# Optimization experiments

Hardware: AMD Instinct MI355X
Metric: run time of the kernel (lower is better)

The kernel has to match this reference:

```python
import jax, jax.numpy as jnp
import numpy as np


def setup_inputs() -> dict:
    key = jax.random.key(0)
    k1, k2 = jax.random.split(key)
    B, Q, P, D = 4, 75, 5, 640  # episodes, queries, prototypes (5-way), feat dim (ResNet-12)
    return {
        "query_feat": jax.random.normal(k1, (B, Q, D), dtype=jnp.float32),
        "proto_feat": jax.random.normal(k2, (B, P, D), dtype=jnp.float32),
    }


def reference(query_feat, proto_feat):
    # Kendall rank correlation (default mode of ProtoLayer).
    # c_pair = combinations(range(D), 2); x[:, c_pair].diff(-1).sign() ==
    # sign(x[..., j] - x[..., i]) for all i < j.
    D = query_feat.shape[-1]
    i_idx, j_idx = np.triu_indices(D, k=1)  # same order as itertools.combinations
    n_pairs = i_idx.shape[0]  # D*(D-1)/2
    q_rank = jnp.sign(query_feat[..., j_idx] - query_feat[..., i_idx])  # (B, Q, n_pairs)
    s_rank = jnp.sign(proto_feat[..., j_idx] - proto_feat[..., i_idx])  # (B, P, n_pairs)
    # per-batch: query_prank @ support_prank.T / n_pairs -> (B, Q, P)
    return jnp.einsum("bqn,bpn->bqp", q_rank, s_rank) / n_pairs
```

## Files before the change

### kernel.cpp

```cpp
#include <hip/hip_runtime.h>
#include <stdint.h>


#define BB 4
#define QQ 75
#define PP 5
#define DD 640
#define NPAIRS 204480
#define NGROUPS 110
#define NROWS_P 20
#define GPW 5

__device__ __forceinline__ void pack_bit(unsigned& w, float xi_t, float xj) {
    asm("v_cmp_lt_f32 vcc, %1, %2\n\t"
        "v_addc_co_u32 %0, vcc, %0, %0, vcc"
        : "+v"(w)
        : "s"(xi_t), "v"(xj)
        : "vcc");
}

__device__ __forceinline__ unsigned pack_word(const float* __restrict__ xi,
                                              float xj, int dlo, int lane) {
    unsigned w0 = 0, w1 = 0, w2 = 0, w3 = 0;
#pragma unroll
    for (int t = 0; t < 8; ++t) {
        pack_bit(w0, xi[t],      xj);
        pack_bit(w1, xi[t + 8],  xj);
        pack_bit(w2, xi[t + 16], xj);
        pack_bit(w3, xi[t + 24], xj);
    }
    unsigned w = (w0 << 24) | (w1 << 16) | (w2 << 8) | w3;
    if (dlo >= 0) {
        const int n = lane - dlo;
        const unsigned msk = (n <= 0) ? 0u
                           : (n >= 32) ? 0xFFFFFFFFu
                                       : (0xFFFFFFFFu << (32 - n));
        w &= msk;
    }
    return w;
}

__device__ __forceinline__ unsigned wave_sum_dpp(unsigned v) {
    v += (unsigned)__builtin_amdgcn_update_dpp(0, (int)v, 0x111, 0xf, 0xf, true);
    v += (unsigned)__builtin_amdgcn_update_dpp(0, (int)v, 0x112, 0xf, 0xf, true);
    v += (unsigned)__builtin_amdgcn_update_dpp(0, (int)v, 0x114, 0xf, 0xf, true);
    v += (unsigned)__builtin_amdgcn_update_dpp(0, (int)v, 0x118, 0xf, 0xf, true);
    v += (unsigned)__builtin_amdgcn_update_dpp(0, (int)v, 0x142, 0xa, 0xf, true);
    v += (unsigned)__builtin_amdgcn_update_dpp(0, (int)v, 0x143, 0xc, 0xf, true);
    return v;
}

__global__ __launch_bounds__(256, 4)
void pack_p(const float* __restrict__ pfeat, unsigned* __restrict__ pm) {
    const int lane = threadIdx.x & 63;
    const int wave = __builtin_amdgcn_readfirstlane(threadIdx.x >> 6);
    const int rp   = blockIdx.x;
    const int G    = blockIdx.y * 4 + wave;
    if (G >= NGROUPS) return;

    int gj = 0;
#pragma unroll 1
    while ((gj + 1) * (gj + 2) <= G) ++gj;
    const int ig = G - gj * (gj + 1);

    const float* __restrict__ row = pfeat + (size_t)rp * DD;
    const float xj = row[64 * gj + lane];
    pm[((size_t)G * NROWS_P + rp) * 64 + lane] =
        pack_word(row + 32 * ig, xj, 32 * ig - 64 * gj, lane);
}

__global__ __launch_bounds__(256, 4)
void kendall(const float* __restrict__ qfeat,
             const unsigned* __restrict__ pm,
             float* __restrict__ out) {
    const int lane = threadIdx.x & 63;
    const int wave = __builtin_amdgcn_readfirstlane(threadIdx.x >> 6);
    const int bq   = blockIdx.x;
    const int slot = blockIdx.y * 4 + wave;
    if (slot >= NGROUPS / GPW) return;
    const int b    = bq / QQ;
    const float* __restrict__ row = qfeat + (size_t)bq * DD;

    const int G0 = GPW * slot;
    int gj = 0;
#pragma unroll 1
    while ((gj + 1) * (gj + 2) <= G0) ++gj;
    int ig = G0 - gj * (gj + 1);

    int gjs[GPW], igs[GPW];
#pragma unroll
    for (int k = 0; k < GPW; ++k) {
        gjs[k] = gj; igs[k] = ig;
        if (++ig == 2 * gj + 2) { ++gj; ig = 0; }
    }

    unsigned pr[GPW][PP];
#pragma unroll
    for (int k = 0; k < GPW; ++k) {
        const unsigned* __restrict__ pw =
            pm + ((size_t)(G0 + k) * NROWS_P + b * PP) * 64 + lane;
#pragma unroll
        for (int p = 0; p < PP; ++p) pr[k][p] = pw[p * 64];
    }

    unsigned m0 = 0, m1 = 0, m2 = 0, m3 = 0, m4 = 0;

#pragma unroll
    for (int k = 0; k < GPW; ++k) {
        const float xj = row[64 * gjs[k] + lane];
        const unsigned qw = pack_word(row + 32 * igs[k], xj,
                                      32 * igs[k] - 64 * gjs[k], lane);
        m0 += __popc(qw ^ pr[k][0]);
        m1 += __popc(qw ^ pr[k][1]);
        m2 += __popc(qw ^ pr[k][2]);
        m3 += __popc(qw ^ pr[k][3]);
        m4 += __popc(qw ^ pr[k][4]);
    }

    const unsigned s01 = wave_sum_dpp(m0 | (m1 << 16));
    const unsigned s23 = wave_sum_dpp(m2 | (m3 << 16));
    const unsigned s4  = wave_sum_dpp(m4);
    const unsigned c01 = (unsigned)__builtin_amdgcn_readlane((int)s01, 63);
    const unsigned c23 = (unsigned)__builtin_amdgcn_readlane((int)s23, 63);
    const unsigned c4  = (unsigned)__builtin_amdgcn_readlane((int)s4,  63);

    if (lane == 0) {
        const float base = (slot == 0) ? 1.0f : 0.0f;
        const float s = -2.0f / (float)NPAIRS;
        float* o = out + (size_t)bq * PP;
        atomicAdd(o + 0, base + s * (float)(c01 & 0xFFFFu));
        atomicAdd(o + 1, base + s * (float)(c01 >> 16));
        atomicAdd(o + 2, base + s * (float)(c23 & 0xFFFFu));
        atomicAdd(o + 3, base + s * (float)(c23 >> 16));
        atomicAdd(o + 4, base + s * (float)c4);
    }
}

extern "C" void kernel_launch(void* const* d_in, const int* in_sizes, int n_in,
                              void* d_out, int out_size, void* d_ws, size_t ws_size,
                              hipStream_t stream) {
    const float* qfeat = (const float*)d_in[0];
    const float* pfeat = (const float*)d_in[1];
    float* out = (float*)d_out;
    unsigned* pm = (unsigned*)d_ws;

    pack_p <<<dim3(NROWS_P, 28), 256, 0, stream>>>(pfeat, pm);
    kendall<<<dim3(BB * QQ, 6),  256, 0, stream>>>(qfeat, pm, out);
}
```

Before: 69.32 us.

## Fuse prototype bit-packing into the Kendall kernel via shared memory

```diff
diff --git a/kernel.cpp b/kernel.cpp
--- a/kernel.cpp
+++ b/kernel.cpp
@@ -8,8 +8,9 @@
 #define DD 640
 #define NPAIRS 204480
 #define NGROUPS 110
-#define NROWS_P 20
 #define GPW 5
+#define NSLOT (NGROUPS / GPW)
+#define QUADS 19
 
 __device__ __forceinline__ void pack_bit(unsigned& w, float xi_t, float xj) {
     asm("v_cmp_lt_f32 vcc, %1, %2\n\t"
@@ -50,43 +51,29 @@
     return v;
 }
 
-__global__ __launch_bounds__(256, 4)
-void pack_p(const float* __restrict__ pfeat, unsigned* __restrict__ pm) {
+__global__ __launch_bounds__(256, 8)
+void kendall_fused(const float* __restrict__ qfeat,
+                   const float* __restrict__ pfeat,
+                   float* __restrict__ out) {
+    __shared__ unsigned plds[GPW * PP * 64];
+
     const int lane = threadIdx.x & 63;
     const int wave = __builtin_amdgcn_readfirstlane(threadIdx.x >> 6);
-    const int rp   = blockIdx.x;
-    const int G    = blockIdx.y * 4 + wave;
-    if (G >= NGROUPS) return;
+    const int b    = blockIdx.x / QUADS;
+    const int quad = blockIdx.x - b * QUADS;
+    const int slot = blockIdx.y;
+    const int G0   = GPW * slot;
 
-    int gj = 0;
-#pragma unroll 1
-    while ((gj + 1) * (gj + 2) <= G) ++gj;
-    const int ig = G - gj * (gj + 1);
-
-    const float* __restrict__ row = pfeat + (size_t)rp * DD;
-    const float xj = row[64 * gj + lane];
-    pm[((size_t)G * NROWS_P + rp) * 64 + lane] =
-        pack_word(row + 32 * ig, xj, 32 * ig - 64 * gj, lane);
-}
-
-__global__ __launch_bounds__(256, 4)
-void kendall(const float* __restrict__ qfeat,
-             const unsigned* __restrict__ pm,
-             float* __restrict__ out) {
-    const int lane = threadIdx.x & 63;
-    const int wave = __builtin_amdgcn_readfirstlane(threadIdx.x >> 6);
-    const int bq   = blockIdx.x;
-    const int slot = blockIdx.y * 4 + wave;
-    if (slot >= NGROUPS / GPW) return;
-    const int b    = bq / QQ;
+    const int lrow   = 4 * quad + wave;
+    const bool active = (lrow < QQ);
+    const int  r      = active ? lrow : (QQ - 1);
+    const int  bq     = b * QQ + r;
     const float* __restrict__ row = qfeat + (size_t)bq * DD;
 
-    const int G0 = GPW * slot;
     int gj = 0;
 #pragma unroll 1
     while ((gj + 1) * (gj + 2) <= G0) ++gj;
     int ig = G0 - gj * (gj + 1);
-
     int gjs[GPW], igs[GPW];
 #pragma unroll
     for (int k = 0; k < GPW; ++k) {
@@ -94,27 +81,66 @@
         if (++ig == 2 * gj + 2) { ++gj; ig = 0; }
     }
 
+    float xj0, xj1, xj2, xj3, xj4;
+    {
+        xj0 = row[64 * gjs[0] + lane];
+        xj1 = row[64 * gjs[1] + lane];
+        xj2 = row[64 * gjs[2] + lane];
+        xj3 = row[64 * gjs[3] + lane];
+        xj4 = row[64 * gjs[4] + lane];
+    }
+
+    const float* __restrict__ pbase = pfeat + (size_t)b * PP * DD;
+#pragma unroll 1
+    for (int widx = wave; widx < GPW * PP; widx += 4) {
+        const int kk = widx / 5;
+        const int p  = widx - kk * 5;
+        const int G  = G0 + kk;
+        int gjw = 0;
+#pragma unroll 1
+        while ((gjw + 1) * (gjw + 2) <= G) ++gjw;
+        const int igw = G - gjw * (gjw + 1);
+        const float* __restrict__ prow = pbase + (size_t)p * DD;
+        plds[widx * 64 + lane] =
+            pack_word(prow + 32 * igw, prow[64 * gjw + lane],
+                      32 * igw - 64 * gjw, lane);
+    }
+    __syncthreads();
+
     unsigned pr[GPW][PP];
 #pragma unroll
-    for (int k = 0; k < GPW; ++k) {
-        const unsigned* __restrict__ pw =
-            pm + ((size_t)(G0 + k) * NROWS_P + b * PP) * 64 + lane;
+    for (int k = 0; k < GPW; ++k)
 #pragma unroll
-        for (int p = 0; p < PP; ++p) pr[k][p] = pw[p * 64];
-    }
+        for (int p = 0; p < PP; ++p)
+            pr[k][p] = plds[(k * PP + p) * 64 + lane];
 
     unsigned m0 = 0, m1 = 0, m2 = 0, m3 = 0, m4 = 0;
-
-#pragma unroll
-    for (int k = 0; k < GPW; ++k) {
-        const float xj = row[64 * gjs[k] + lane];
-        const unsigned qw = pack_word(row + 32 * igs[k], xj,
-                                      32 * igs[k] - 64 * gjs[k], lane);
-        m0 += __popc(qw ^ pr[k][0]);
-        m1 += __popc(qw ^ pr[k][1]);
-        m2 += __popc(qw ^ pr[k][2]);
-        m3 += __popc(qw ^ pr[k][3]);
-        m4 += __popc(qw ^ pr[k][4]);
+    {
+        const unsigned qw0 = pack_word(row + 32 * igs[0], xj0,
+                                       32 * igs[0] - 64 * gjs[0], lane);
+        m0 += __popc(qw0 ^ pr[0][0]); m1 += __popc(qw0 ^ pr[0][1]);
+        m2 += __popc(qw0 ^ pr[0][2]); m3 += __popc(qw0 ^ pr[0][3]);
+        m4 += __popc(qw0 ^ pr[0][4]);
+        const unsigned qw1 = pack_word(row + 32 * igs[1], xj1,
+                                       32 * igs[1] - 64 * gjs[1], lane);
+        m0 += __popc(qw1 ^ pr[1][0]); m1 += __popc(qw1 ^ pr[1][1]);
+        m2 += __popc(qw1 ^ pr[1][2]); m3 += __popc(qw1 ^ pr[1][3]);
+        m4 += __popc(qw1 ^ pr[1][4]);
+        const unsigned qw2 = pack_word(row + 32 * igs[2], xj2,
+                                       32 * igs[2] - 64 * gjs[2], lane);
+        m0 += __popc(qw2 ^ pr[2][0]); m1 += __popc(qw2 ^ pr[2][1]);
+        m2 += __popc(qw2 ^ pr[2][2]); m3 += __popc(qw2 ^ pr[2][3]);
+        m4 += __popc(qw2 ^ pr[2][4]);
+        const unsigned qw3 = pack_word(row + 32 * igs[3], xj3,
+                                       32 * igs[3] - 64 * gjs[3], lane);
+        m0 += __popc(qw3 ^ pr[3][0]); m1 += __popc(qw3 ^ pr[3][1]);
+        m2 += __popc(qw3 ^ pr[3][2]); m3 += __popc(qw3 ^ pr[3][3]);
+        m4 += __popc(qw3 ^ pr[3][4]);
+        const unsigned qw4 = pack_word(row + 32 * igs[4], xj4,
+                                       32 * igs[4] - 64 * gjs[4], lane);
+        m0 += __popc(qw4 ^ pr[4][0]); m1 += __popc(qw4 ^ pr[4][1]);
+        m2 += __popc(qw4 ^ pr[4][2]); m3 += __popc(qw4 ^ pr[4][3]);
+        m4 += __popc(qw4 ^ pr[4][4]);
     }
 
     const unsigned s01 = wave_sum_dpp(m0 | (m1 << 16));
@@ -124,7 +150,7 @@
     const unsigned c23 = (unsigned)__builtin_amdgcn_readlane((int)s23, 63);
     const unsigned c4  = (unsigned)__builtin_amdgcn_readlane((int)s4,  63);
 
-    if (lane == 0) {
+    if (lane == 0 && active) {
         const float base = (slot == 0) ? 1.0f : 0.0f;
         const float s = -2.0f / (float)NPAIRS;
         float* o = out + (size_t)bq * PP;
@@ -142,8 +168,7 @@
     const float* qfeat = (const float*)d_in[0];
     const float* pfeat = (const float*)d_in[1];
     float* out = (float*)d_out;
-    unsigned* pm = (unsigned*)d_ws;
+    (void)d_ws; (void)ws_size;
 
-    pack_p <<<dim3(NROWS_P, 28), 256, 0, stream>>>(pfeat, pm);
-    kendall<<<dim3(BB * QQ, 6),  256, 0, stream>>>(qfeat, pm, out);
+    kendall_fused<<<dim3(BB * QUADS, NSLOT), 256, 0, stream>>>(qfeat, pfeat, out);
 }
```

Measured after the change: 70.59 us. About the same (+1.8%).
